# Kernel tuning notes

Hardware: AMD Instinct MI355X
Metric: run time of the kernel (lower is better)

## Reference

```python
import jax, jax.numpy as jnp
import numpy as np

SCALING = 2.0  # alpha / rank = 16 / 8


def _kron(A, B):
    # A: (m, n), B: (p, q) -> (m*p, n*q), same broadcast-multiply-reshape as torch code
    m, n = A.shape
    p, q = B.shape
    return (A[:, None, :, None] * B[None, :, None, :]).reshape(m * p, n * q)


def setup_inputs() -> dict:
    key = jax.random.key(0)
    k1, k2, k3, k4 = jax.random.split(key, 4)
    x = jax.random.normal(k1, (128, 8192), dtype=jnp.float32)
    original_weight = jax.random.normal(k2, (8192, 8192), dtype=jnp.float32) * 0.02
    lokr_A = jax.random.normal(k3, (512, 8192), dtype=jnp.float32) * 0.02
    lokr_B = jax.random.normal(k4, (16, 1), dtype=jnp.float32) * 0.02
    scalar = jnp.ones((1,), dtype=jnp.float32)
    return {"x": x, "original_weight": original_weight, "lokr_A": lokr_A,
            "lokr_B": lokr_B, "scalar": scalar}


def reference(x, original_weight, lokr_A, lokr_B, scalar):
    # delta_W = (A kron B) * scaling ; W_eff = W + scalar * delta_W ; out = x @ W_eff^T
    delta_W = _kron(lokr_A, lokr_B) * SCALING          # (8192, 8192)
    W_eff = original_weight + scalar[0] * delta_W      # bypass_mode with original weight
    return x @ W_eff.T                                 # dropout=0 -> identity
```

## Files before the change

### kernel.cpp

```cpp
#include <hip/hip_runtime.h>


#define M_DIM 128
#define N_DIM 8192
#define K_DIM 8192
#define BN 128
#define BK 64
#define KSPLIT 8
#define KCHUNK (K_DIM / KSPLIT)

typedef __attribute__((ext_vector_type(8))) short bf16x8;
typedef __attribute__((ext_vector_type(4))) float f32x4;

__device__ __forceinline__ unsigned short f2bf(float f) {
  unsigned u = __builtin_bit_cast(unsigned, f);
  u += 0x7FFFu + ((u >> 16) & 1u);
  return (unsigned short)(u >> 16);
}

__global__ void convert_x_kernel(const float4* __restrict__ x4,
                                 ushort4* __restrict__ xb4) {
  int t = blockIdx.x * blockDim.x + threadIdx.x;
  const int n4 = M_DIM * K_DIM / 4;
  for (int i = t; i < n4; i += gridDim.x * blockDim.x) {
    float4 v = x4[i];
    ushort4 o;
    o.x = f2bf(v.x); o.y = f2bf(v.y); o.z = f2bf(v.z); o.w = f2bf(v.w);
    xb4[i] = o;
  }
}

__global__ __launch_bounds__(256, 2) void lokr_main(
    const float* __restrict__ W,
    const float* __restrict__ A,
    const float* __restrict__ Bv,
    const float* __restrict__ scal,
    const unsigned short* __restrict__ xb,
    float* __restrict__ part)
{
  __shared__ unsigned short bs[144][BK + 8];

  const int t    = threadIdx.x;
  const int lane = t & 63;
  const int wv   = t >> 6;
  const int bx   = blockIdx.x;
  const int ks   = bx & (KSPLIT - 1);
  const int ntb  = bx >> 3;
  const int r0   = ntb * BN;
  const int i0   = ntb * (BN / 16);
  const int kbase = ks * KCHUNK;
  const int tr = t >> 4, tc = t & 15;

  const float sB = 2.0f * scal[0] * Bv[lane & 15];

  f32x4 accW[2][8];
  f32x4 accY[2];
  const f32x4 z4 = {0.f, 0.f, 0.f, 0.f};
#pragma unroll
  for (int a = 0; a < 2; ++a) {
    accY[a] = z4;
#pragma unroll
    for (int b = 0; b < 8; ++b) accW[a][b] = z4;
  }

  const float* Wrow = W + (size_t)(r0 + tr) * K_DIM + kbase + tc * 4;
  const float* Arow = A + (size_t)(i0 + (tr & 7)) * K_DIM + kbase + tc * 4;
  const bool aact = (tr < 8);
  const unsigned short* xcol = xb + kbase;

  float4 wreg[8];
  float4 areg;
#pragma unroll
  for (int j = 0; j < 8; ++j)
    wreg[j] = *(const float4*)(Wrow + (size_t)j * 16 * K_DIM);
  if (aact) areg = *(const float4*)Arow;
  else      { areg.x = areg.y = areg.z = areg.w = 0.f; }

  for (int kt = 0; kt < KCHUNK; kt += BK) {
#pragma unroll
    for (int j = 0; j < 8; ++j) {
      ushort4 o;
      o.x = f2bf(wreg[j].x); o.y = f2bf(wreg[j].y);
      o.z = f2bf(wreg[j].z); o.w = f2bf(wreg[j].w);
      *(ushort4*)&bs[j * 16 + tr][tc * 4] = o;
    }
    {
      ushort4 o;
      o.x = f2bf(areg.x); o.y = f2bf(areg.y);
      o.z = f2bf(areg.z); o.w = f2bf(areg.w);
      *(ushort4*)&bs[128 + tr][tc * 4] = o;
    }
    __syncthreads();

    if (kt + BK < KCHUNK) {
#pragma unroll
      for (int j = 0; j < 8; ++j)
        wreg[j] = *(const float4*)(Wrow + (size_t)j * 16 * K_DIM + kt + BK);
      if (aact) areg = *(const float4*)(Arow + kt + BK);
    }

    bf16x8 af[2][2];
#pragma unroll
    for (int kk = 0; kk < 2; ++kk) {
      const int koff = kk * 32 + (lane >> 4) * 8;
#pragma unroll
      for (int mt = 0; mt < 2; ++mt)
        af[kk][mt] = *(const bf16x8*)(xcol +
            (size_t)(wv * 32 + mt * 16 + (lane & 15)) * K_DIM + kt + koff);
    }
#pragma unroll
    for (int kk = 0; kk < 2; ++kk) {
      const int koff = kk * 32 + (lane >> 4) * 8;
#pragma unroll
      for (int n9 = 0; n9 < 9; ++n9) {
        bf16x8 bf = *(const bf16x8*)&bs[n9 * 16 + (lane & 15)][koff];
#pragma unroll
        for (int mt = 0; mt < 2; ++mt) {
          if (n9 < 8)
            accW[mt][n9] = __builtin_amdgcn_mfma_f32_16x16x32_bf16(af[kk][mt], bf, accW[mt][n9], 0, 0, 0);
          else
            accY[mt] = __builtin_amdgcn_mfma_f32_16x16x32_bf16(af[kk][mt], bf, accY[mt], 0, 0, 0);
        }
      }
    }
    __syncthreads();
  }

  float* p = part + (size_t)ks * M_DIM * N_DIM;
#pragma unroll
  for (int mt = 0; mt < 2; ++mt) {
#pragma unroll
    for (int n9 = 0; n9 < 8; ++n9) {
      int srcl = (lane & 48) | n9;
#pragma unroll
      for (int reg = 0; reg < 4; ++reg) {
        float y2v = __shfl(accY[mt][reg], srcl, 64);
        int m = wv * 32 + mt * 16 + (lane >> 4) * 4 + reg;
        int r = r0 + n9 * 16 + (lane & 15);
        p[(size_t)m * N_DIM + r] = accW[mt][n9][reg] + sB * y2v;
      }
    }
  }
}

__global__ void reduce_kernel(const float4* __restrict__ part,
                              float4* __restrict__ out) {
  int t = blockIdx.x * blockDim.x + threadIdx.x;
  const int n4 = M_DIM * N_DIM / 4;
  for (int i = t; i < n4; i += gridDim.x * blockDim.x) {
    float4 s = part[i];
#pragma unroll
    for (int ksp = 1; ksp < KSPLIT; ++ksp) {
      float4 v = part[(size_t)ksp * n4 + i];
      s.x += v.x; s.y += v.y; s.z += v.z; s.w += v.w;
    }
    out[i] = s;
  }
}

extern "C" void kernel_launch(void* const* d_in, const int* in_sizes, int n_in,
                              void* d_out, int out_size, void* d_ws, size_t ws_size,
                              hipStream_t stream) {
  const float* x    = (const float*)d_in[0];
  const float* W    = (const float*)d_in[1];
  const float* A    = (const float*)d_in[2];
  const float* Bv   = (const float*)d_in[3];
  const float* scal = (const float*)d_in[4];
  float* out = (float*)d_out;

  unsigned short* xb = (unsigned short*)d_ws;
  float* part = (float*)((char*)d_ws + (size_t)M_DIM * K_DIM * sizeof(unsigned short));

  convert_x_kernel<<<512, 256, 0, stream>>>((const float4*)x, (ushort4*)xb);
  lokr_main<<<(N_DIM / BN) * KSPLIT, 256, 0, stream>>>(W, A, Bv, scal, xb, part);
  reduce_kernel<<<1024, 256, 0, stream>>>((const float4*)part, (float4*)out);
}
```

Measured before the change: 414.1 us.

## Split K across waves in-block and reduce via LDS, drop partial-sum kernel

Restructures the main GEMM so each 512-thread block owns 32 output columns and all 128 rows, with the eight waves splitting K and loading W/A fragments straight into registers (converted to bf16) instead of staging them through LDS. The partial sums are reduced in shared memory and written directly to the output, which removes the 8-way split-K partial buffer in global memory and the separate reduce kernel. In exchange, each wave rereads x from global/L2 for every block, the grid shrinks to 256 blocks, and register pressure from 24 accumulators per lane rises.

After: 454.5 us. 1.1x slower.

```diff
diff --git a/kernel.cpp b/kernel.cpp
--- a/kernel.cpp
+++ b/kernel.cpp
@@ -4,10 +4,9 @@
 #define M_DIM 128
 #define N_DIM 8192
 #define K_DIM 8192
-#define BN 128
-#define BK 64
-#define KSPLIT 8
-#define KCHUNK (K_DIM / KSPLIT)
+#define BN 32
+#define NWAVE 8
+#define KW (K_DIM / NWAVE)
 
 typedef __attribute__((ext_vector_type(8))) short bf16x8;
 typedef __attribute__((ext_vector_type(4))) float f32x4;
@@ -16,6 +15,15 @@
   unsigned u = __builtin_bit_cast(unsigned, f);
   u += 0x7FFFu + ((u >> 16) & 1u);
   return (unsigned short)(u >> 16);
+}
+
+__device__ __forceinline__ bf16x8 cvt8(float4 a, float4 b) {
+  bf16x8 r;
+  r[0] = (short)f2bf(a.x); r[1] = (short)f2bf(a.y);
+  r[2] = (short)f2bf(a.z); r[3] = (short)f2bf(a.w);
+  r[4] = (short)f2bf(b.x); r[5] = (short)f2bf(b.y);
+  r[6] = (short)f2bf(b.z); r[7] = (short)f2bf(b.w);
+  return r;
 }
 
 __global__ void convert_x_kernel(const float4* __restrict__ x4,
@@ -30,131 +38,119 @@
   }
 }
 
-__global__ __launch_bounds__(256, 2) void lokr_main(
+__global__ __launch_bounds__(512, 2) void lokr_main(
     const float* __restrict__ W,
     const float* __restrict__ A,
     const float* __restrict__ Bv,
     const float* __restrict__ scal,
     const unsigned short* __restrict__ xb,
-    float* __restrict__ part)
+    float* __restrict__ out)
 {
-  __shared__ unsigned short bs[144][BK + 8];
+  __shared__ float red[NWAVE * M_DIM * 16];
 
   const int t    = threadIdx.x;
   const int lane = t & 63;
   const int wv   = t >> 6;
-  const int bx   = blockIdx.x;
-  const int ks   = bx & (KSPLIT - 1);
-  const int ntb  = bx >> 3;
-  const int r0   = ntb * BN;
-  const int i0   = ntb * (BN / 16);
-  const int kbase = ks * KCHUNK;
-  const int tr = t >> 4, tc = t & 15;
+  const int b    = blockIdx.x;
+  const int l15  = lane & 15;
+  const int l4   = lane >> 4;
+  const int kw   = wv * KW;
 
-  const float sB = 2.0f * scal[0] * Bv[lane & 15];
+  const float sB = 2.0f * scal[0] * Bv[l15];
 
-  f32x4 accW[2][8];
-  f32x4 accY[2];
+  f32x4 accW[8][2];
+  f32x4 accY[8];
   const f32x4 z4 = {0.f, 0.f, 0.f, 0.f};
 #pragma unroll
-  for (int a = 0; a < 2; ++a) {
-    accY[a] = z4;
-#pragma unroll
-    for (int b = 0; b < 8; ++b) accW[a][b] = z4;
+  for (int mf = 0; mf < 8; ++mf) {
+    accY[mf] = z4;
+    accW[mf][0] = z4;
+    accW[mf][1] = z4;
   }
 
-  const float* Wrow = W + (size_t)(r0 + tr) * K_DIM + kbase + tc * 4;
-  const float* Arow = A + (size_t)(i0 + (tr & 7)) * K_DIM + kbase + tc * 4;
-  const bool aact = (tr < 8);
-  const unsigned short* xcol = xb + kbase;
+  const float* Wp = W + (size_t)(b * BN + l15) * K_DIM + kw + l4 * 8;
+  const float* Ap = A + (size_t)(2 * b + (l15 >> 3)) * K_DIM + kw + l4 * 8;
+  const unsigned short* xp = xb + (size_t)l15 * K_DIM + kw + l4 * 8;
 
-  float4 wreg[8];
-  float4 areg;
+  float4 wr[2][2][2];
+  float4 ar[2][2];
 #pragma unroll
-  for (int j = 0; j < 8; ++j)
-    wreg[j] = *(const float4*)(Wrow + (size_t)j * 16 * K_DIM);
-  if (aact) areg = *(const float4*)Arow;
-  else      { areg.x = areg.y = areg.z = areg.w = 0.f; }
+  for (int nf = 0; nf < 2; ++nf)
+#pragma unroll
+    for (int kk = 0; kk < 2; ++kk)
+#pragma unroll
+      for (int h = 0; h < 2; ++h)
+        wr[nf][kk][h] = *(const float4*)(Wp + (size_t)nf * 16 * K_DIM + kk * 32 + h * 4);
+#pragma unroll
+  for (int kk = 0; kk < 2; ++kk)
+#pragma unroll
+    for (int h = 0; h < 2; ++h)
+      ar[kk][h] = *(const float4*)(Ap + kk * 32 + h * 4);
 
-  for (int kt = 0; kt < KCHUNK; kt += BK) {
+  for (int kt = 0; kt < KW; kt += 64) {
+    bf16x8 wbf[2][2], abf[2];
 #pragma unroll
-    for (int j = 0; j < 8; ++j) {
-      ushort4 o;
-      o.x = f2bf(wreg[j].x); o.y = f2bf(wreg[j].y);
-      o.z = f2bf(wreg[j].z); o.w = f2bf(wreg[j].w);
-      *(ushort4*)&bs[j * 16 + tr][tc * 4] = o;
-    }
-    {
-      ushort4 o;
-      o.x = f2bf(areg.x); o.y = f2bf(areg.y);
-      o.z = f2bf(areg.z); o.w = f2bf(areg.w);
-      *(ushort4*)&bs[128 + tr][tc * 4] = o;
-    }
-    __syncthreads();
+    for (int nf = 0; nf < 2; ++nf)
+#pragma unroll
+      for (int kk = 0; kk < 2; ++kk)
+        wbf[nf][kk] = cvt8(wr[nf][kk][0], wr[nf][kk][1]);
+#pragma unroll
+    for (int kk = 0; kk < 2; ++kk)
+      abf[kk] = cvt8(ar[kk][0], ar[kk][1]);
 
-    if (kt + BK < KCHUNK) {
+    if (kt + 64 < KW) {
 #pragma unroll
-      for (int j = 0; j < 8; ++j)
-        wreg[j] = *(const float4*)(Wrow + (size_t)j * 16 * K_DIM + kt + BK);
-      if (aact) areg = *(const float4*)(Arow + kt + BK);
+      for (int nf = 0; nf < 2; ++nf)
+#pragma unroll
+        for (int kk = 0; kk < 2; ++kk)
+#pragma unroll
+          for (int h = 0; h < 2; ++h)
+            wr[nf][kk][h] = *(const float4*)(Wp + (size_t)nf * 16 * K_DIM + kt + 64 + kk * 32 + h * 4);
+#pragma unroll
+      for (int kk = 0; kk < 2; ++kk)
+#pragma unroll
+        for (int h = 0; h < 2; ++h)
+          ar[kk][h] = *(const float4*)(Ap + kt + 64 + kk * 32 + h * 4);
     }
 
-    bf16x8 af[2][2];
 #pragma unroll
     for (int kk = 0; kk < 2; ++kk) {
-      const int koff = kk * 32 + (lane >> 4) * 8;
+      bf16x8 xa[8];
 #pragma unroll
-      for (int mt = 0; mt < 2; ++mt)
-        af[kk][mt] = *(const bf16x8*)(xcol +
-            (size_t)(wv * 32 + mt * 16 + (lane & 15)) * K_DIM + kt + koff);
+      for (int mf = 0; mf < 8; ++mf)
+        xa[mf] = *(const bf16x8*)(xp + (size_t)mf * 16 * K_DIM + kt + kk * 32);
+#pragma unroll
+      for (int mf = 0; mf < 8; ++mf) {
+        accW[mf][0] = __builtin_amdgcn_mfma_f32_16x16x32_bf16(xa[mf], wbf[0][kk], accW[mf][0], 0, 0, 0);
+        accW[mf][1] = __builtin_amdgcn_mfma_f32_16x16x32_bf16(xa[mf], wbf[1][kk], accW[mf][1], 0, 0, 0);
+        accY[mf]    = __builtin_amdgcn_mfma_f32_16x16x32_bf16(xa[mf], abf[kk],    accY[mf],    0, 0, 0);
+      }
     }
+  }
+
+#pragma unroll 1
+  for (int nf = 0; nf < 2; ++nf) {
+    if (nf) __syncthreads();
 #pragma unroll
-    for (int kk = 0; kk < 2; ++kk) {
-      const int koff = kk * 32 + (lane >> 4) * 8;
+    for (int mf = 0; mf < 8; ++mf) {
 #pragma unroll
-      for (int n9 = 0; n9 < 9; ++n9) {
-        bf16x8 bf = *(const bf16x8*)&bs[n9 * 16 + (lane & 15)][koff];
-#pragma unroll
-        for (int mt = 0; mt < 2; ++mt) {
-          if (n9 < 8)
-            accW[mt][n9] = __builtin_amdgcn_mfma_f32_16x16x32_bf16(af[kk][mt], bf, accW[mt][n9], 0, 0, 0);
-          else
-            accY[mt] = __builtin_amdgcn_mfma_f32_16x16x32_bf16(af[kk][mt], bf, accY[mt], 0, 0, 0);
-        }
+      for (int r = 0; r < 4; ++r) {
+        float y2v = __shfl(accY[mf][r], (lane & 48) | (nf << 3), 64);
+        int m = mf * 16 + l4 * 4 + r;
+        red[wv * 2048 + m * 16 + l15] = accW[mf][nf][r] + sB * y2v;
       }
     }
     __syncthreads();
-  }
-
-  float* p = part + (size_t)ks * M_DIM * N_DIM;
+    const float* rp = red + t * 4;
+    float4 s = *(const float4*)rp;
 #pragma unroll
-  for (int mt = 0; mt < 2; ++mt) {
-#pragma unroll
-    for (int n9 = 0; n9 < 8; ++n9) {
-      int srcl = (lane & 48) | n9;
-#pragma unroll
-      for (int reg = 0; reg < 4; ++reg) {
-        float y2v = __shfl(accY[mt][reg], srcl, 64);
-        int m = wv * 32 + mt * 16 + (lane >> 4) * 4 + reg;
-        int r = r0 + n9 * 16 + (lane & 15);
-        p[(size_t)m * N_DIM + r] = accW[mt][n9][reg] + sB * y2v;
-      }
-    }
-  }
-}
-
-__global__ void reduce_kernel(const float4* __restrict__ part,
-                              float4* __restrict__ out) {
-  int t = blockIdx.x * blockDim.x + threadIdx.x;
-  const int n4 = M_DIM * N_DIM / 4;
-  for (int i = t; i < n4; i += gridDim.x * blockDim.x) {
-    float4 s = part[i];
-#pragma unroll
-    for (int ksp = 1; ksp < KSPLIT; ++ksp) {
-      float4 v = part[(size_t)ksp * n4 + i];
+    for (int w = 1; w < NWAVE; ++w) {
+      float4 v = *(const float4*)(rp + w * 2048);
       s.x += v.x; s.y += v.y; s.z += v.z; s.w += v.w;
     }
-    out[i] = s;
+    int m  = t >> 2;
+    int c0 = (t & 3) * 4;
+    *(float4*)(out + (size_t)m * N_DIM + b * BN + nf * 16 + c0) = s;
   }
 }
 
@@ -169,9 +165,7 @@
   float* out = (float*)d_out;
 
   unsigned short* xb = (unsigned short*)d_ws;
-  float* part = (float*)((char*)d_ws + (size_t)M_DIM * K_DIM * sizeof(unsigned short));
 
   convert_x_kernel<<<512, 256, 0, stream>>>((const float4*)x, (ushort4*)xb);
-  lokr_main<<<(N_DIM / BN) * KSPLIT, 256, 0, stream>>>(W, A, Bv, scal, xb, part);
-  reduce_kernel<<<1024, 256, 0, stream>>>((const float4*)part, (float4*)out);
+  lokr_main<<<N_DIM / BN, 512, 0, stream>>>(W, A, Bv, scal, xb, out);
 }
```
